# Optimization experiments

Hardware: AMD Instinct MI355X
Metric: run time of the kernel (lower is better)

## Reference

```python
import jax, jax.numpy as jnp
import numpy as np

EPS = 1e-7

def fake_quant(x, bits):
    """Per-tensor affine fake-quantization (dnn-gating TorchRoundToBits),
    matching torch.fake_quantize_per_tensor_affine with dynamic range."""
    fp_max = jax.lax.stop_gradient(jnp.max(x))
    fp_min = jax.lax.stop_gradient(jnp.min(x))
    qmax = float(2 ** bits - 1)
    qmin = 0.0
    scale = (fp_max - fp_min) / (qmax - qmin) + EPS
    zero_point = jnp.trunc(qmin - fp_min / scale)  # int() cast in torch truncates
    q = jnp.round(x / scale + zero_point)
    qc = jnp.clip(q, qmin, qmax)
    return (qc - zero_point) * scale

def conv2d(x, w, stride=1, padding=1):
    return jax.lax.conv_general_dilated(
        x, w,
        window_strides=(stride, stride),
        padding=[(padding, padding), (padding, padding)],
        dimension_numbers=('NCHW', 'OIHW', 'NCHW'))

def setup_inputs() -> dict:
    key = jax.random.key(0)
    k1, k2 = jax.random.split(key)
    x = jax.random.normal(k1, (32, 256, 56, 56), dtype=jnp.float32)
    # kaiming-like init for a 3x3 conv with 256 in-channels
    fan_in = 256 * 3 * 3
    weight = jax.random.normal(k2, (256, 256, 3, 3), dtype=jnp.float32) / np.sqrt(fan_in)
    return {"x": x, "weight": weight}

def reference(x, weight):
    WBITS, ABITS, PGABITS = 8, 8, 4
    TH = 0.99
    w_q = fake_quant(weight, WBITS)          # quantized weights (shared by both convs)
    msb_in = fake_quant(x, PGABITS)          # low-precision (MSB) input
    msb_out = conv2d(msb_in, w_q)            # [32,256,56,56] prediction pass
    lsb_in = fake_quant(x, ABITS) - msb_in   # residual (LSB) input
    lsb_out = conv2d(lsb_in, w_q)            # high-precision correction pass
    mask = (jax.nn.sigmoid(msb_out) > TH).astype(msb_out.dtype)
    return msb_out + mask * lsb_out
```

## Files before the change

kernel.cpp:

```cpp
#include <hip/hip_runtime.h>
#include <stdint.h>
#include <stddef.h>

typedef int v4i  __attribute__((ext_vector_type(4)));
typedef int v16i __attribute__((ext_vector_type(16)));

struct QParams {
  float s4, z4, s8, z8, sw, zw;
  float s4sw, s8sw;
  int dw;
};

__device__ __forceinline__ unsigned enc_f(float f) {
  unsigned u = __float_as_uint(f);
  return (u & 0x80000000u) ? ~u : (u | 0x80000000u);
}
__device__ __forceinline__ float dec_f(unsigned e) {
  unsigned u = (e & 0x80000000u) ? (e ^ 0x80000000u) : ~e;
  return __uint_as_float(u);
}

__global__ void k_init(unsigned* mm, unsigned* zp) {
  int t = threadIdx.x;
  if (t < 128) zp[t] = 0u;
  if (t == 0) { mm[0] = 0xFFFFFFFFu; mm[1] = 0u; mm[2] = 0xFFFFFFFFu; mm[3] = 0u; }
}

__global__ void k_minmax(const float4* __restrict__ p, int n4, unsigned* mm) {
  float lmin = 3.4e38f, lmax = -3.4e38f;
  for (int i = blockIdx.x * blockDim.x + threadIdx.x; i < n4; i += gridDim.x * blockDim.x) {
    float4 v = p[i];
    lmin = fminf(lmin, fminf(fminf(v.x, v.y), fminf(v.z, v.w)));
    lmax = fmaxf(lmax, fmaxf(fmaxf(v.x, v.y), fmaxf(v.z, v.w)));
  }
  for (int off = 32; off; off >>= 1) {
    lmin = fminf(lmin, __shfl_down(lmin, off, 64));
    lmax = fmaxf(lmax, __shfl_down(lmax, off, 64));
  }
  __shared__ float smin[4], smax[4];
  int w = threadIdx.x >> 6, lane = threadIdx.x & 63;
  if (lane == 0) { smin[w] = lmin; smax[w] = lmax; }
  __syncthreads();
  if (threadIdx.x == 0) {
    float a = fminf(fminf(smin[0], smin[1]), fminf(smin[2], smin[3]));
    float b = fmaxf(fmaxf(smax[0], smax[1]), fmaxf(smax[2], smax[3]));
    atomicMin(&mm[0], enc_f(a));
    atomicMax(&mm[1], enc_f(b));
  }
}

__global__ void k_params(const unsigned* mm, QParams* q) {
  float xmin = dec_f(mm[0]), xmax = dec_f(mm[1]);
  float wmin = dec_f(mm[2]), wmax = dec_f(mm[3]);
  float s4 = (xmax - xmin) / 15.0f + 1e-7f;
  float z4 = truncf(0.0f - xmin / s4);
  float s8 = (xmax - xmin) / 255.0f + 1e-7f;
  float z8 = truncf(0.0f - xmin / s8);
  float sw = (wmax - wmin) / 255.0f + 1e-7f;
  float zw = truncf(0.0f - wmin / sw);
  q->s4 = s4; q->z4 = z4; q->s8 = s8; q->z8 = z8; q->sw = sw; q->zw = zw;
  q->s4sw = s4 * sw; q->s8sw = s8 * sw;
  q->dw = 128 - (int)zw;
}

__global__ void k_quant_w(const float* __restrict__ w, const QParams* __restrict__ q,
                          char* __restrict__ Wc) {
  int t = blockIdx.x * 256 + threadIdx.x;
  float sw = q->sw, zw = q->zw;
  const float* src = w + (size_t)t * 9;
#pragma unroll
  for (int j = 0; j < 9; ++j) {
    float qf = rintf(__fdiv_rn(src[j], sw) + zw);
    qf = fminf(fmaxf(qf, 0.0f), 255.0f);
    Wc[j * 65536 + t] = (char)((int)qf - 128);
  }
}

__global__ void k_quant_x(const float* __restrict__ x, const QParams* __restrict__ q,
                          char* __restrict__ A4, char* __restrict__ A8,
                          int* __restrict__ CS4, int* __restrict__ CS8) {
  __shared__ char sm4[56 * 257];
  __shared__ char sm8[56 * 257];
  __shared__ int cp4[56][4], cp8[56][4];
  int bx = blockIdx.x;
  int n = bx / 56, y = bx % 56;
  int tid = threadIdx.x;
  float s4 = q->s4, z4 = q->z4, s8 = q->s8, z8 = q->z8;
  const float* xrow = x + (size_t)n * 802816 + y * 56;
#pragma unroll 2
  for (int it = 0; it < 56; ++it) {
    int idx = it * 256 + tid;
    int c = idx / 56, xc = idx % 56;
    float v = xrow[(size_t)c * 3136 + xc];
    float q4 = rintf(__fdiv_rn(v, s4) + z4);
    q4 = fminf(fmaxf(q4, 0.0f), 15.0f);
    int t4 = (int)(q4 - z4);
    float q8 = rintf(__fdiv_rn(v, s8) + z8);
    q8 = fminf(fmaxf(q8, 0.0f), 255.0f);
    int t8 = (int)(q8 - z8);
    t8 = max(-128, min(127, t8));
    sm4[xc * 257 + c] = (char)t4;
    sm8[xc * 257 + c] = (char)t8;
  }
  __syncthreads();
  if (tid < 224) {
    int xc = tid >> 2, qq = tid & 3;
    const char* r4 = sm4 + xc * 257 + qq * 64;
    const char* r8 = sm8 + xc * 257 + qq * 64;
    int a = 0, b = 0;
#pragma unroll 8
    for (int c = 0; c < 64; ++c) { a += (signed char)r4[c]; b += (signed char)r8[c]; }
    cp4[xc][qq] = a; cp8[xc][qq] = b;
  }
  __syncthreads();
  int pixbase = n * 3136 + y * 56;
  if (tid < 56) {
    CS4[pixbase + tid] = cp4[tid][0] + cp4[tid][1] + cp4[tid][2] + cp4[tid][3];
    CS8[pixbase + tid] = cp8[tid][0] + cp8[tid][1] + cp8[tid][2] + cp8[tid][3];
  }
  unsigned* A4w = (unsigned*)A4;
  unsigned* A8w = (unsigned*)A8;
#pragma unroll 2
  for (int it = 0; it < 14; ++it) {
    int idx = it * 256 + tid;
    int xc = idx >> 6, wd = idx & 63;
    int sb = xc * 257 + wd * 4;
    unsigned u4 = (unsigned)(unsigned char)sm4[sb]
                | ((unsigned)(unsigned char)sm4[sb + 1] << 8)
                | ((unsigned)(unsigned char)sm4[sb + 2] << 16)
                | ((unsigned)(unsigned char)sm4[sb + 3] << 24);
    unsigned u8 = (unsigned)(unsigned char)sm8[sb]
                | ((unsigned)(unsigned char)sm8[sb + 1] << 8)
                | ((unsigned)(unsigned char)sm8[sb + 2] << 16)
                | ((unsigned)(unsigned char)sm8[sb + 3] << 24);
    size_t o = (size_t)(pixbase + xc) * 64 + wd;
    A4w[o] = u4; A8w[o] = u8;
  }
}

__global__ void k_wsum(const int* __restrict__ CS4, const int* __restrict__ CS8,
                       int* __restrict__ S4, int* __restrict__ S8) {
  int p = blockIdx.x * 256 + threadIdx.x;
  if (p >= 100352) return;
  int rem = p % 3136;
  int y = rem / 56, xc = rem % 56;
  int a = 0, b = 0;
#pragma unroll
  for (int dy = -1; dy <= 1; ++dy) {
    if ((unsigned)(y + dy) >= 56u) continue;
#pragma unroll
    for (int dx = -1; dx <= 1; ++dx) {
      if ((unsigned)(xc + dx) >= 56u) continue;
      int qq = p + dy * 56 + dx;
      a += CS4[qq]; b += CS8[qq];
    }
  }
  S4[p] = a; S8[p] = b;
}

#define GLD16(gp, lp)                                                         \
  __builtin_amdgcn_global_load_lds((const __attribute__((address_space(1))) void*)(gp), \
                                   (__attribute__((address_space(3))) void*)(lp), 16, 0, 0)

__device__ __forceinline__ float pg_merge(int a4v, int a8v, float fs4, float fs8) {
  float msb = fs4 * (float)a4v;
  float c8  = fs8 * (float)a8v;
  float lsb = c8 - msb;
  float sig = 1.0f / (1.0f + expf(-msb));
  return msb + (sig > 0.99f ? lsb : 0.0f);
}

__global__ __launch_bounds__(256, 2) void k_conv(
    const char* __restrict__ A4, const char* __restrict__ A8,
    const char* __restrict__ Wc,
    const int* __restrict__ S4, const int* __restrict__ S8,
    const QParams* __restrict__ q, const char* __restrict__ zpage,
    float* __restrict__ out) {
  __shared__ char smA4[8192], smA8[8192], smB[8192];
  const size_t ASZ = 25690112;
  int tid = threadIdx.x;
  int w = tid >> 6, lane = tid & 63;
  int m0 = blockIdx.x * 128;
  int n0 = blockIdx.y * 128;
  int wm = w >> 1, wn = w & 1;

  int chunk = lane & 3;
  int r0 = (w << 5) + (lane >> 2);
  int r1 = r0 + 16;
  int cg0 = chunk ^ ((r0 >> 1) & 3);
  int cg1 = chunk ^ ((r1 >> 1) & 3);
  int p0 = m0 + r0, p1 = m0 + r1;
  int rem0 = p0 % 3136, rem1 = p1 % 3136;
  int y0 = rem0 / 56, x0 = rem0 % 56;
  int y1 = rem1 / 56, x1 = rem1 % 56;
  const char* aBase0 = A4 + (size_t)p0 * 256 + cg0 * 16;
  const char* aBase1 = A4 + (size_t)p1 * 256 + cg1 * 16;
  const char* bBase0 = Wc + (n0 + r0) * 256 + cg0 * 16;
  const char* bBase1 = Wc + (n0 + r1) * 256 + cg1 * 16;
  const char* zp0 = zpage + chunk * 16;

  char* dA4 = smA4 + (w << 11);
  char* dA8 = smA8 + (w << 11);
  char* dB  = smB  + (w << 11);

  v16i acc4[2][2] = {}, acc8[2][2] = {};
  int r31 = lane & 31, qh = lane >> 5;

  for (int win = 0; win < 9; ++win) {
    int dy = win / 3 - 1, dx = win % 3 - 1;
    int doff = (dy * 56 + dx) * 256;
    bool v0ok = ((unsigned)(y0 + dy) < 56u) && ((unsigned)(x0 + dx) < 56u);
    bool v1ok = ((unsigned)(y1 + dy) < 56u) && ((unsigned)(x1 + dx) < 56u);
    const char* g40 = v0ok ? aBase0 + doff : zp0;
    const char* g41 = v1ok ? aBase1 + doff : zp0;
    const char* g80 = v0ok ? aBase0 + doff + ASZ : zp0;
    const char* g81 = v1ok ? aBase1 + doff + ASZ : zp0;
    const char* gB0 = bBase0 + win * 65536;
    const char* gB1 = bBase1 + win * 65536;
#pragma unroll
    for (int cs = 0; cs < 4; ++cs) {
      int c0 = cs * 64;
      GLD16(g40 + c0, dA4);
      GLD16(g41 + c0, dA4 + 1024);
      GLD16(g80 + c0, dA8);
      GLD16(g81 + c0, dA8 + 1024);
      GLD16(gB0 + c0, dB);
      GLD16(gB1 + c0, dB + 1024);
      asm volatile("s_waitcnt vmcnt(0)" ::: "memory");
      __syncthreads();
#pragma unroll
      for (int kc = 0; kc < 2; ++kc) {
        int ch = kc * 2 + qh;
        v4i a4f[2], a8f[2], bf[2];
#pragma unroll
        for (int fm = 0; fm < 2; ++fm) {
          int row = wm * 64 + fm * 32 + r31;
          int off = row * 64 + ((ch ^ ((row >> 1) & 3)) << 4);
          a4f[fm] = *(const v4i*)(smA4 + off);
          a8f[fm] = *(const v4i*)(smA8 + off);
        }
#pragma unroll
        for (int fn = 0; fn < 2; ++fn) {
          int row = wn * 64 + fn * 32 + r31;
          int off = row * 64 + ((ch ^ ((row >> 1) & 3)) << 4);
          bf[fn] = *(const v4i*)(smB + off);
        }
#pragma unroll
        for (int fm = 0; fm < 2; ++fm)
#pragma unroll
          for (int fn = 0; fn < 2; ++fn) {
            acc4[fm][fn] = __builtin_amdgcn_mfma_i32_32x32x32_i8(a4f[fm], bf[fn], acc4[fm][fn], 0, 0, 0);
            acc8[fm][fn] = __builtin_amdgcn_mfma_i32_32x32x32_i8(a8f[fm], bf[fn], acc8[fm][fn], 0, 0, 0);
          }
      }
      __syncthreads();
    }
  }

  float fs4 = q->s4sw, fs8 = q->s8sw;
  int dwv = q->dw;
#pragma unroll
  for (int fm = 0; fm < 2; ++fm)
#pragma unroll
    for (int fn = 0; fn < 2; ++fn) {
      int kout = n0 + wn * 64 + fn * 32 + r31;
      int pb = m0 + wm * 64 + fm * 32 + 4 * qh;
#pragma unroll
      for (int rg = 0; rg < 4; ++rg) {
        int pr = pb + 8 * rg;
        int4 sv4 = *(const int4*)(S4 + pr);
        int4 sv8 = *(const int4*)(S8 + pr);
        float4 res;
        res.x = pg_merge(acc4[fm][fn][rg * 4 + 0] + dwv * sv4.x,
                         acc8[fm][fn][rg * 4 + 0] + dwv * sv8.x, fs4, fs8);
        res.y = pg_merge(acc4[fm][fn][rg * 4 + 1] + dwv * sv4.y,
                         acc8[fm][fn][rg * 4 + 1] + dwv * sv8.y, fs4, fs8);
        res.z = pg_merge(acc4[fm][fn][rg * 4 + 2] + dwv * sv4.z,
                         acc8[fm][fn][rg * 4 + 2] + dwv * sv8.z, fs4, fs8);
        res.w = pg_merge(acc4[fm][fn][rg * 4 + 3] + dwv * sv4.w,
                         acc8[fm][fn][rg * 4 + 3] + dwv * sv8.w, fs4, fs8);
        int nimg = pr / 3136;
        int rem = pr - nimg * 3136;
        *(float4*)(out + (size_t)nimg * 802816 + (size_t)kout * 3136 + rem) = res;
      }
    }
}

extern "C" void kernel_launch(void* const* d_in, const int* in_sizes, int n_in,
                              void* d_out, int out_size, void* d_ws, size_t ws_size,
                              hipStream_t stream) {
  const float* x  = (const float*)d_in[0];
  const float* wt = (const float*)d_in[1];
  float* out = (float*)d_out;

  char* ws = (char*)d_ws;
  unsigned* mm = (unsigned*)ws;
  QParams* prm = (QParams*)(ws + 64);
  char* zpage = ws + 256;
  char* A4 = ws + 1024;
  const size_t ASZ = 25690112;
  char* A8 = A4 + ASZ;
  int* CS4 = (int*)(A8 + ASZ);
  int* CS8 = CS4 + 100352;
  int* S4  = CS8 + 100352;
  int* S8  = S4 + 100352;
  char* Wc = (char*)(S8 + 100352);

  k_init<<<1, 256, 0, stream>>>(mm, (unsigned*)zpage);
  k_minmax<<<1024, 256, 0, stream>>>((const float4*)x, 25690112 / 4, mm);
  k_minmax<<<64, 256, 0, stream>>>((const float4*)wt, 589824 / 4, mm + 2);
  k_params<<<1, 1, 0, stream>>>(mm, prm);
  k_quant_w<<<256, 256, 0, stream>>>(wt, prm, Wc);
  k_quant_x<<<1792, 256, 0, stream>>>(x, prm, A4, A8, CS4, CS8);
  k_wsum<<<392, 256, 0, stream>>>(CS4, CS8, S4, S8);
  k_conv<<<dim3(784, 2), 256, 0, stream>>>(A4, A8, Wc, S4, S8, prm, zpage, out);
}
```

Before: 429.2 us.

## Load A fragments directly to registers in MFMA layout and double-buffer weight tiles

The quantized activations are rewritten into a fragment-native layout (32-pixel by 16-channel blocks), so the conv kernel can load A operands straight from global memory into registers instead of staging them through LDS. Only the weights go through LDS, now double-buffered, and the loads for the next k-step are issued before the current step's MFMAs, giving one barrier per step. Each wave now owns 32 pixel rows by 128 outputs. The quant kernels are also vectorized (float4 input reads, word-wise byte sums, coalesced weight stores), and the zero page moves to the end of each activation buffer. The trade-off is higher register pressure from the register-held fragments and less reuse of A across waves, so each A fragment is re-read from global or cache.

After: 425.9 us. Within noise of the previous version (-0.8%).

```diff
diff --git a/kernel.cpp b/kernel.cpp
--- a/kernel.cpp
+++ b/kernel.cpp
@@ -20,10 +20,12 @@
   return __uint_as_float(u);
 }
 
-__global__ void k_init(unsigned* mm, unsigned* zp) {
+__global__ void k_init(unsigned* mm, uint4* t4, uint4* t8) {
   int t = threadIdx.x;
-  if (t < 128) zp[t] = 0u;
   if (t == 0) { mm[0] = 0xFFFFFFFFu; mm[1] = 0u; mm[2] = 0xFFFFFFFFu; mm[3] = 0u; }
+  uint4 z; z.x = z.y = z.z = z.w = 0u;
+  t4[t] = z; t4[t + 256] = z;
+  t8[t] = z; t8[t + 256] = z;
 }
 
 __global__ void k_minmax(const float4* __restrict__ p, int n4, unsigned* mm) {
@@ -65,52 +67,83 @@
 
 __global__ void k_quant_w(const float* __restrict__ w, const QParams* __restrict__ q,
                           char* __restrict__ Wc) {
-  int t = blockIdx.x * 256 + threadIdx.x;
+  __shared__ char sm[2304];
+  int b = blockIdx.x;
+  int tid = threadIdx.x;
   float sw = q->sw, zw = q->zw;
-  const float* src = w + (size_t)t * 9;
+  const float* src = w + (size_t)b * 2304;
 #pragma unroll
   for (int j = 0; j < 9; ++j) {
-    float qf = rintf(__fdiv_rn(src[j], sw) + zw);
+    int o = j * 256 + tid;
+    float qf = rintf(__fdiv_rn(src[o], sw) + zw);
     qf = fminf(fmaxf(qf, 0.0f), 255.0f);
-    Wc[j * 65536 + t] = (char)((int)qf - 128);
-  }
-}
-
-__global__ void k_quant_x(const float* __restrict__ x, const QParams* __restrict__ q,
+    int c = o / 9, jj = o - c * 9;
+    sm[jj * 256 + c] = (char)((int)qf - 128);
+  }
+  __syncthreads();
+  if (tid < 64) {
+#pragma unroll
+    for (int j = 0; j < 9; ++j)
+      *(unsigned*)(Wc + (size_t)j * 65536 + b * 256 + tid * 4) =
+          *(const unsigned*)(sm + j * 256 + tid * 4);
+  }
+}
+
+__device__ __forceinline__ void quant2(float v, float s4, float z4, float s8, float z8,
+                                       char& o4, char& o8) {
+  float q4 = rintf(__fdiv_rn(v, s4) + z4);
+  q4 = fminf(fmaxf(q4, 0.0f), 15.0f);
+  o4 = (char)(int)(q4 - z4);
+  float q8 = rintf(__fdiv_rn(v, s8) + z8);
+  q8 = fminf(fmaxf(q8, 0.0f), 255.0f);
+  int t8 = (int)(q8 - z8);
+  o8 = (char)max(-128, min(127, t8));
+}
+
+__device__ __forceinline__ int bsum4(int u) {
+  return (int)(signed char)(u & 0xff) + (int)(signed char)((u >> 8) & 0xff)
+       + (int)(signed char)((u >> 16) & 0xff) + (int)(signed char)((u >> 24) & 0xff);
+}
+
+__global__ void k_quant_x(const float4* __restrict__ x4, const QParams* __restrict__ q,
                           char* __restrict__ A4, char* __restrict__ A8,
                           int* __restrict__ CS4, int* __restrict__ CS8) {
-  __shared__ char sm4[56 * 257];
-  __shared__ char sm8[56 * 257];
+  __shared__ __align__(16) char sm4[56 * 256];
+  __shared__ __align__(16) char sm8[56 * 256];
   __shared__ int cp4[56][4], cp8[56][4];
   int bx = blockIdx.x;
   int n = bx / 56, y = bx % 56;
   int tid = threadIdx.x;
   float s4 = q->s4, z4 = q->z4, s8 = q->s8, z8 = q->z8;
-  const float* xrow = x + (size_t)n * 802816 + y * 56;
+  const float4* xrow = x4 + (size_t)n * 200704 + y * 14;
 #pragma unroll 2
-  for (int it = 0; it < 56; ++it) {
+  for (int it = 0; it < 14; ++it) {
     int idx = it * 256 + tid;
-    int c = idx / 56, xc = idx % 56;
-    float v = xrow[(size_t)c * 3136 + xc];
-    float q4 = rintf(__fdiv_rn(v, s4) + z4);
-    q4 = fminf(fmaxf(q4, 0.0f), 15.0f);
-    int t4 = (int)(q4 - z4);
-    float q8 = rintf(__fdiv_rn(v, s8) + z8);
-    q8 = fminf(fmaxf(q8, 0.0f), 255.0f);
-    int t8 = (int)(q8 - z8);
-    t8 = max(-128, min(127, t8));
-    sm4[xc * 257 + c] = (char)t4;
-    sm8[xc * 257 + c] = (char)t8;
+    int c = idx / 14, xq = idx - c * 14;
+    float4 v = xrow[(size_t)c * 784 + xq];
+    int c16 = c >> 4, cl = c & 15;
+    int px0 = xq * 4;
+    int s0 = px0 & 15;
+    char a0, b0; quant2(v.x, s4, z4, s8, z8, a0, b0);
+    char a1, b1; quant2(v.y, s4, z4, s8, z8, a1, b1);
+    char a2, b2; quant2(v.z, s4, z4, s8, z8, a2, b2);
+    char a3, b3; quant2(v.w, s4, z4, s8, z8, a3, b3);
+    int d0 = (px0 + 0) * 256 + ((c16 ^ (s0 + 0)) << 4) + cl;
+    int d1 = (px0 + 1) * 256 + ((c16 ^ (s0 + 1)) << 4) + cl;
+    int d2 = (px0 + 2) * 256 + ((c16 ^ (s0 + 2)) << 4) + cl;
+    int d3 = (px0 + 3) * 256 + ((c16 ^ (s0 + 3)) << 4) + cl;
+    sm4[d0] = a0; sm4[d1] = a1; sm4[d2] = a2; sm4[d3] = a3;
+    sm8[d0] = b0; sm8[d1] = b1; sm8[d2] = b2; sm8[d3] = b3;
   }
   __syncthreads();
   if (tid < 224) {
-    int xc = tid >> 2, qq = tid & 3;
-    const char* r4 = sm4 + xc * 257 + qq * 64;
-    const char* r8 = sm8 + xc * 257 + qq * 64;
+    int px = tid >> 2, qq = tid & 3;
+    const int* r4 = (const int*)(sm4 + px * 256 + qq * 64);
+    const int* r8 = (const int*)(sm8 + px * 256 + qq * 64);
     int a = 0, b = 0;
-#pragma unroll 8
-    for (int c = 0; c < 64; ++c) { a += (signed char)r4[c]; b += (signed char)r8[c]; }
-    cp4[xc][qq] = a; cp8[xc][qq] = b;
+#pragma unroll
+    for (int j = 0; j < 16; ++j) { a += bsum4(r4[j]); b += bsum4(r8[j]); }
+    cp4[px][qq] = a; cp8[px][qq] = b;
   }
   __syncthreads();
   int pixbase = n * 3136 + y * 56;
@@ -118,23 +151,19 @@
     CS4[pixbase + tid] = cp4[tid][0] + cp4[tid][1] + cp4[tid][2] + cp4[tid][3];
     CS8[pixbase + tid] = cp8[tid][0] + cp8[tid][1] + cp8[tid][2] + cp8[tid][3];
   }
-  unsigned* A4w = (unsigned*)A4;
-  unsigned* A8w = (unsigned*)A8;
-#pragma unroll 2
-  for (int it = 0; it < 14; ++it) {
+#pragma unroll
+  for (int it = 0; it < 4; ++it) {
     int idx = it * 256 + tid;
-    int xc = idx >> 6, wd = idx & 63;
-    int sb = xc * 257 + wd * 4;
-    unsigned u4 = (unsigned)(unsigned char)sm4[sb]
-                | ((unsigned)(unsigned char)sm4[sb + 1] << 8)
-                | ((unsigned)(unsigned char)sm4[sb + 2] << 16)
-                | ((unsigned)(unsigned char)sm4[sb + 3] << 24);
-    unsigned u8 = (unsigned)(unsigned char)sm8[sb]
-                | ((unsigned)(unsigned char)sm8[sb + 1] << 8)
-                | ((unsigned)(unsigned char)sm8[sb + 2] << 16)
-                | ((unsigned)(unsigned char)sm8[sb + 3] << 24);
-    size_t o = (size_t)(pixbase + xc) * 64 + wd;
-    A4w[o] = u4; A8w[o] = u8;
+    if (idx < 896) {
+      int c16 = idx / 56, xc = idx - c16 * 56;
+      int so = xc * 256 + ((c16 ^ (xc & 15)) << 4);
+      v4i v4v = *(const v4i*)(sm4 + so);
+      v4i v8v = *(const v4i*)(sm8 + so);
+      int pg = pixbase + xc;
+      size_t o = (size_t)(pg >> 5) * 8192 + (size_t)c16 * 512 + (size_t)(pg & 31) * 16;
+      *(v4i*)(A4 + o) = v4v;
+      *(v4i*)(A8 + o) = v8v;
+    }
   }
 }
 
@@ -170,120 +199,128 @@
   return msb + (sig > 0.99f ? lsb : 0.0f);
 }
 
+struct Frag { v4i a4k0, a4k1, a8k0, a8k1; };
+
+#define ISSUE(S, DB, F)                                                        \
+  {                                                                            \
+    const int s_ = (S);                                                        \
+    const int win_ = s_ >> 2;                                                  \
+    const int cs_ = s_ & 3;                                                    \
+    const char* bsrc_ = gB + win_ * 65536 + cs_ * 64;                          \
+    GLD16(bsrc_, (DB));                                                        \
+    GLD16(bsrc_ + 4096, (DB) + 1024);                                          \
+    unsigned ao_ = vofs[win_] + (unsigned)(cs_ << 11);                         \
+    (F).a4k0 = *(const v4i*)(A4 + ao_);                                        \
+    (F).a4k1 = *(const v4i*)(A4 + ao_ + 1024);                                 \
+    (F).a8k0 = *(const v4i*)(A8 + ao_);                                        \
+    (F).a8k1 = *(const v4i*)(A8 + ao_ + 1024);                                 \
+  }
+
+#define COMPUTE(BUF, F)                                                        \
+  {                                                                            \
+    _Pragma("unroll")                                                          \
+    for (int kc = 0; kc < 2; ++kc) {                                           \
+      v4i bf[4];                                                               \
+      _Pragma("unroll")                                                        \
+      for (int fn = 0; fn < 4; ++fn)                                           \
+        bf[fn] = *(const v4i*)((const char*)smB + (BUF) * 8192 + offB[fn][kc]);\
+      v4i a4_ = kc ? (F).a4k1 : (F).a4k0;                                      \
+      v4i a8_ = kc ? (F).a8k1 : (F).a8k0;                                      \
+      _Pragma("unroll")                                                        \
+      for (int fn = 0; fn < 4; ++fn) {                                         \
+        acc4[fn] = __builtin_amdgcn_mfma_i32_32x32x32_i8(a4_, bf[fn], acc4[fn], 0, 0, 0); \
+        acc8[fn] = __builtin_amdgcn_mfma_i32_32x32x32_i8(a8_, bf[fn], acc8[fn], 0, 0, 0); \
+      }                                                                        \
+    }                                                                          \
+  }
+
 __global__ __launch_bounds__(256, 2) void k_conv(
     const char* __restrict__ A4, const char* __restrict__ A8,
     const char* __restrict__ Wc,
     const int* __restrict__ S4, const int* __restrict__ S8,
-    const QParams* __restrict__ q, const char* __restrict__ zpage,
+    const QParams* __restrict__ q,
     float* __restrict__ out) {
-  __shared__ char smA4[8192], smA8[8192], smB[8192];
-  const size_t ASZ = 25690112;
+  __shared__ char smB[2][8192];
+  const unsigned ASZ = 25690112u;
   int tid = threadIdx.x;
   int w = tid >> 6, lane = tid & 63;
+  int l31 = lane & 31, qh = lane >> 5;
   int m0 = blockIdx.x * 128;
   int n0 = blockIdx.y * 128;
-  int wm = w >> 1, wn = w & 1;
-
-  int chunk = lane & 3;
-  int r0 = (w << 5) + (lane >> 2);
-  int r1 = r0 + 16;
-  int cg0 = chunk ^ ((r0 >> 1) & 3);
-  int cg1 = chunk ^ ((r1 >> 1) & 3);
-  int p0 = m0 + r0, p1 = m0 + r1;
-  int rem0 = p0 % 3136, rem1 = p1 % 3136;
-  int y0 = rem0 / 56, x0 = rem0 % 56;
-  int y1 = rem1 / 56, x1 = rem1 % 56;
-  const char* aBase0 = A4 + (size_t)p0 * 256 + cg0 * 16;
-  const char* aBase1 = A4 + (size_t)p1 * 256 + cg1 * 16;
-  const char* bBase0 = Wc + (n0 + r0) * 256 + cg0 * 16;
-  const char* bBase1 = Wc + (n0 + r1) * 256 + cg1 * 16;
-  const char* zp0 = zpage + chunk * 16;
-
-  char* dA4 = smA4 + (w << 11);
-  char* dA8 = smA8 + (w << 11);
-  char* dB  = smB  + (w << 11);
-
-  v16i acc4[2][2] = {}, acc8[2][2] = {};
-  int r31 = lane & 31, qh = lane >> 5;
-
+
+  int p = m0 + w * 32 + l31;
+  int rem = p % 3136;
+  int y = rem / 56, x = rem % 56;
+  unsigned zoff = ASZ + (unsigned)(qh * 512 + l31 * 16);
+  unsigned vofs[9];
+#pragma unroll
   for (int win = 0; win < 9; ++win) {
     int dy = win / 3 - 1, dx = win % 3 - 1;
-    int doff = (dy * 56 + dx) * 256;
-    bool v0ok = ((unsigned)(y0 + dy) < 56u) && ((unsigned)(x0 + dx) < 56u);
-    bool v1ok = ((unsigned)(y1 + dy) < 56u) && ((unsigned)(x1 + dx) < 56u);
-    const char* g40 = v0ok ? aBase0 + doff : zp0;
-    const char* g41 = v1ok ? aBase1 + doff : zp0;
-    const char* g80 = v0ok ? aBase0 + doff + ASZ : zp0;
-    const char* g81 = v1ok ? aBase1 + doff + ASZ : zp0;
-    const char* gB0 = bBase0 + win * 65536;
-    const char* gB1 = bBase1 + win * 65536;
-#pragma unroll
-    for (int cs = 0; cs < 4; ++cs) {
-      int c0 = cs * 64;
-      GLD16(g40 + c0, dA4);
-      GLD16(g41 + c0, dA4 + 1024);
-      GLD16(g80 + c0, dA8);
-      GLD16(g81 + c0, dA8 + 1024);
-      GLD16(gB0 + c0, dB);
-      GLD16(gB1 + c0, dB + 1024);
-      asm volatile("s_waitcnt vmcnt(0)" ::: "memory");
-      __syncthreads();
-#pragma unroll
-      for (int kc = 0; kc < 2; ++kc) {
-        int ch = kc * 2 + qh;
-        v4i a4f[2], a8f[2], bf[2];
-#pragma unroll
-        for (int fm = 0; fm < 2; ++fm) {
-          int row = wm * 64 + fm * 32 + r31;
-          int off = row * 64 + ((ch ^ ((row >> 1) & 3)) << 4);
-          a4f[fm] = *(const v4i*)(smA4 + off);
-          a8f[fm] = *(const v4i*)(smA8 + off);
-        }
-#pragma unroll
-        for (int fn = 0; fn < 2; ++fn) {
-          int row = wn * 64 + fn * 32 + r31;
-          int off = row * 64 + ((ch ^ ((row >> 1) & 3)) << 4);
-          bf[fn] = *(const v4i*)(smB + off);
-        }
-#pragma unroll
-        for (int fm = 0; fm < 2; ++fm)
-#pragma unroll
-          for (int fn = 0; fn < 2; ++fn) {
-            acc4[fm][fn] = __builtin_amdgcn_mfma_i32_32x32x32_i8(a4f[fm], bf[fn], acc4[fm][fn], 0, 0, 0);
-            acc8[fm][fn] = __builtin_amdgcn_mfma_i32_32x32x32_i8(a8f[fm], bf[fn], acc8[fm][fn], 0, 0, 0);
-          }
-      }
-      __syncthreads();
+    bool ok = ((unsigned)(y + dy) < 56u) && ((unsigned)(x + dx) < 56u);
+    int mp = p + dy * 56 + dx;
+    vofs[win] = ok ? ((((unsigned)mp >> 5) << 13) | ((unsigned)qh << 9) |
+                     (((unsigned)mp & 31u) << 4))
+                   : zoff;
+  }
+
+  int r0 = w * 32 + (lane >> 2);
+  int chunk = lane & 3;
+  int cg = chunk ^ ((r0 >> 1) & 3);
+  const char* gB = Wc + (n0 + r0) * 256 + cg * 16;
+  char* dB0 = &smB[0][w * 2048];
+  char* dB1 = &smB[1][w * 2048];
+
+  int offB[4][2];
+#pragma unroll
+  for (int fn = 0; fn < 4; ++fn) {
+    int row = fn * 32 + l31;
+    int swz = (row >> 1) & 3;
+#pragma unroll
+    for (int kc = 0; kc < 2; ++kc)
+      offB[fn][kc] = row * 64 + (((kc * 2 + qh) ^ swz) << 4);
+  }
+
+  v16i acc4[4] = {}, acc8[4] = {};
+  Frag F0, F1;
+
+  ISSUE(0, dB0, F0);
+  __syncthreads();
+#pragma unroll
+  for (int s = 0; s < 36; ++s) {
+    if (s + 1 < 36) {
+      if ((s & 1) == 0) { ISSUE(s + 1, dB1, F1); }
+      else              { ISSUE(s + 1, dB0, F0); }
     }
+    if ((s & 1) == 0) { COMPUTE(0, F0); }
+    else              { COMPUTE(1, F1); }
+    __syncthreads();
   }
 
   float fs4 = q->s4sw, fs8 = q->s8sw;
   int dwv = q->dw;
-#pragma unroll
-  for (int fm = 0; fm < 2; ++fm)
-#pragma unroll
-    for (int fn = 0; fn < 2; ++fn) {
-      int kout = n0 + wn * 64 + fn * 32 + r31;
-      int pb = m0 + wm * 64 + fm * 32 + 4 * qh;
-#pragma unroll
-      for (int rg = 0; rg < 4; ++rg) {
-        int pr = pb + 8 * rg;
-        int4 sv4 = *(const int4*)(S4 + pr);
-        int4 sv8 = *(const int4*)(S8 + pr);
-        float4 res;
-        res.x = pg_merge(acc4[fm][fn][rg * 4 + 0] + dwv * sv4.x,
-                         acc8[fm][fn][rg * 4 + 0] + dwv * sv8.x, fs4, fs8);
-        res.y = pg_merge(acc4[fm][fn][rg * 4 + 1] + dwv * sv4.y,
-                         acc8[fm][fn][rg * 4 + 1] + dwv * sv8.y, fs4, fs8);
-        res.z = pg_merge(acc4[fm][fn][rg * 4 + 2] + dwv * sv4.z,
-                         acc8[fm][fn][rg * 4 + 2] + dwv * sv8.z, fs4, fs8);
-        res.w = pg_merge(acc4[fm][fn][rg * 4 + 3] + dwv * sv4.w,
-                         acc8[fm][fn][rg * 4 + 3] + dwv * sv8.w, fs4, fs8);
-        int nimg = pr / 3136;
-        int rem = pr - nimg * 3136;
-        *(float4*)(out + (size_t)nimg * 802816 + (size_t)kout * 3136 + rem) = res;
-      }
+  int pb = m0 + w * 32 + 4 * qh;
+#pragma unroll
+  for (int fn = 0; fn < 4; ++fn) {
+    int kout = n0 + fn * 32 + l31;
+#pragma unroll
+    for (int rg = 0; rg < 4; ++rg) {
+      int pr = pb + 8 * rg;
+      int4 sv4 = *(const int4*)(S4 + pr);
+      int4 sv8 = *(const int4*)(S8 + pr);
+      float4 res;
+      res.x = pg_merge(acc4[fn][rg * 4 + 0] + dwv * sv4.x,
+                       acc8[fn][rg * 4 + 0] + dwv * sv8.x, fs4, fs8);
+      res.y = pg_merge(acc4[fn][rg * 4 + 1] + dwv * sv4.y,
+                       acc8[fn][rg * 4 + 1] + dwv * sv8.y, fs4, fs8);
+      res.z = pg_merge(acc4[fn][rg * 4 + 2] + dwv * sv4.z,
+                       acc8[fn][rg * 4 + 2] + dwv * sv8.z, fs4, fs8);
+      res.w = pg_merge(acc4[fn][rg * 4 + 3] + dwv * sv4.w,
+                       acc8[fn][rg * 4 + 3] + dwv * sv8.w, fs4, fs8);
+      int nimg = pr / 3136;
+      int rr = pr - nimg * 3136;
+      *(float4*)(out + (size_t)nimg * 802816 + (size_t)kout * 3136 + rr) = res;
     }
+  }
 }
 
 extern "C" void kernel_launch(void* const* d_in, const int* in_sizes, int n_in,
@@ -296,22 +333,21 @@
   char* ws = (char*)d_ws;
   unsigned* mm = (unsigned*)ws;
   QParams* prm = (QParams*)(ws + 64);
-  char* zpage = ws + 256;
   char* A4 = ws + 1024;
   const size_t ASZ = 25690112;
-  char* A8 = A4 + ASZ;
-  int* CS4 = (int*)(A8 + ASZ);
+  char* A8 = A4 + ASZ + 8192;
+  int* CS4 = (int*)(A8 + ASZ + 8192);
   int* CS8 = CS4 + 100352;
   int* S4  = CS8 + 100352;
   int* S8  = S4 + 100352;
   char* Wc = (char*)(S8 + 100352);
 
-  k_init<<<1, 256, 0, stream>>>(mm, (unsigned*)zpage);
+  k_init<<<1, 256, 0, stream>>>(mm, (uint4*)(A4 + ASZ), (uint4*)(A8 + ASZ));
   k_minmax<<<1024, 256, 0, stream>>>((const float4*)x, 25690112 / 4, mm);
   k_minmax<<<64, 256, 0, stream>>>((const float4*)wt, 589824 / 4, mm + 2);
   k_params<<<1, 1, 0, stream>>>(mm, prm);
   k_quant_w<<<256, 256, 0, stream>>>(wt, prm, Wc);
-  k_quant_x<<<1792, 256, 0, stream>>>(x, prm, A4, A8, CS4, CS8);
+  k_quant_x<<<1792, 256, 0, stream>>>((const float4*)x, prm, A4, A8, CS4, CS8);
   k_wsum<<<392, 256, 0, stream>>>(CS4, CS8, S4, S8);
-  k_conv<<<dim3(784, 2), 256, 0, stream>>>(A4, A8, Wc, S4, S8, prm, zpage, out);
-}
+  k_conv<<<dim3(784, 2), 256, 0, stream>>>(A4, A8, Wc, S4, S8, prm, out);
+}
```
